# Kernel tuning notes

Hardware: AMD Instinct MI355X
Metric: run time of the kernel (lower is better)

## Reference

```python
import jax, jax.numpy as jnp
import numpy as np
from jax import lax

NUM_SKETCH = 3
BN_EPS = 1e-5


def setup_inputs() -> dict:
    key = jax.random.key(0)
    ks = jax.random.split(key, 8)
    B, C, H, W = 32, 128, 64, 64
    D = C // 4  # comp_rate = 4
    k = 3
    x = jax.random.normal(ks[0], (B, C, H, W), dtype=jnp.float32)
    fan = C * k * k
    w1 = jax.random.normal(ks[1], (C, C, k, k), dtype=jnp.float32) / np.sqrt(fan)
    w2 = jax.random.normal(ks[2], (C, C, k, k), dtype=jnp.float32) / np.sqrt(fan)
    gamma1 = jnp.ones((C,), jnp.float32); beta1 = jnp.zeros((C,), jnp.float32)
    gamma2 = jnp.ones((C,), jnp.float32); beta2 = jnp.zeros((C,), jnp.float32)
    # count-sketch hash matrices: hs[j] is (D, C), each column c has a single 1
    idx = jax.random.randint(ks[3], (NUM_SKETCH, C), 0, D)
    hs = jax.nn.one_hot(idx, D, dtype=jnp.float32).transpose(0, 2, 1)  # (3, D, C)
    ss = (jax.random.randint(ks[4], (NUM_SKETCH, C), 0, 2) * 2 - 1).astype(jnp.float32)  # (3, C) signs
    return {"x": x, "w1": w1, "w2": w2, "gamma1": gamma1, "beta1": beta1,
            "gamma2": gamma2, "beta2": beta2, "hs": hs, "ss": ss}


def _sketch_conv_unsketch(x, w, hs, ss):
    # w: (Co, Ci, k, k); hs: (J, D, Co); ss: (J, Co)
    Co, Ci, k, _ = w.shape
    J, D, _ = hs.shape
    B, _, H, W = x.shape
    wf = w.reshape(Co, -1)  # (Co, M)
    # sketched weights per sketch j: h_j @ (wf * s_j[:, None])
    w_sk = jnp.einsum('jdc,jc,cm->jdm', hs, ss, wf).reshape(J * D, Ci, k, k)
    # one conv with J*D output channels (padding=1, stride=1 hardcoded in source)
    y = lax.conv_general_dilated(x, w_sk, window_strides=(1, 1),
                                 padding=[(1, 1), (1, 1)],
                                 dimension_numbers=('NCHW', 'OIHW', 'NCHW'))
    y = y.reshape(B, J, D, H, W)
    # unsketch activations: h_j^T @ y_j, then sign scale (num_s=1 so inner median is identity)
    y_un = jnp.einsum('jdc,bjdhw->jbchw', hs, y) * ss[:, None, :, None, None]
    return jnp.median(y_un, axis=0)  # median over the 3 sketches -> (B, Co, H, W)


def _bn_relu(y, gamma, beta):
    # BatchNorm2d in training mode: biased batch stats over (N, H, W)
    mean = jnp.mean(y, axis=(0, 2, 3), keepdims=True)
    var = jnp.var(y, axis=(0, 2, 3), keepdims=True)
    yhat = (y - mean) * lax.rsqrt(var + BN_EPS)
    return jax.nn.relu(yhat * gamma[None, :, None, None] + beta[None, :, None, None])


def reference(x, w1, w2, gamma1, beta1, gamma2, beta2, hs, ss):
    residual = x
    out1 = _bn_relu(_sketch_conv_unsketch(x, w1, hs, ss), gamma1, beta1)
    del out1  # faithful to source bug: second conv loop uses x, discarding out1
    out = _bn_relu(_sketch_conv_unsketch(x, w2, hs, ss), gamma2, beta2)
    return out + residual
```

## Files before the change

### kernel.cpp

```cpp
#include <hip/hip_runtime.h>
#include <stdint.h>

typedef __bf16 bf16x8 __attribute__((ext_vector_type(8)));
typedef float  f32x4  __attribute__((ext_vector_type(4)));

static constexpr int Bn = 32, Cn = 128, Hn = 64, Wn = 64, HWn = 4096;
static constexpr size_t OFF_XT    = 0;
static constexpr size_t OFF_WF    = 33554432;
static constexpr size_t OFF_IDX   = 33775616;
static constexpr size_t OFF_M     = 33777152;
static constexpr size_t OFF_STATS = 67331584;
static constexpr size_t OFF_ZERO  = 67364352;

__device__ __forceinline__ unsigned short f32_to_bf16(float f) {
    union { float f; unsigned u; } v; v.f = f;
    unsigned u = v.u;
    return (unsigned short)((u + 0x7FFFu + ((u >> 16) & 1u)) >> 16);
}
__device__ __forceinline__ float bf16_to_f32(unsigned short h) {
    union { unsigned u; float f; } v; v.u = ((unsigned)h) << 16;
    return v.f;
}
__device__ __forceinline__ float bf_lo(unsigned w) {
    union { unsigned u; float f; } v; v.u = w << 16; return v.f;
}
__device__ __forceinline__ float bf_hi(unsigned w) {
    union { unsigned u; float f; } v; v.u = w & 0xffff0000u; return v.f;
}
__device__ __forceinline__ float med3(float z0, float z1, float z2) {
    float lo = fminf(z0, z1), hi = fmaxf(z0, z1);
    return fmaxf(lo, fminf(hi, z2));
}
__device__ __forceinline__ void gload_lds16(const unsigned short* g, unsigned short* l) {
    __builtin_amdgcn_global_load_lds(
        (const __attribute__((address_space(1))) unsigned int*)(const void*)g,
        (__attribute__((address_space(3))) unsigned int*)(void*)l,
        16, 0, 0);
}

__global__ __launch_bounds__(256) void k_prep(const float* __restrict__ x,
                                              unsigned short* __restrict__ xT,
                                              const float* __restrict__ w2,
                                              const float* __restrict__ hs,
                                              const float* __restrict__ ss,
                                              unsigned short* __restrict__ wf,
                                              int* __restrict__ idx,
                                              float* __restrict__ stats32,
                                              float* __restrict__ zerop) {
    __shared__ __align__(16) unsigned char smraw[20480];
    int t = threadIdx.x;
    if (blockIdx.x < 432) {
        int*   idxs = (int*)smraw;
        float* sss  = (float*)(smraw + 1536);
        for (int i = t; i < 384; i += 256) {
            int j = i >> 7, c = i & 127;
            int found = 0;
#pragma unroll
            for (int d = 0; d < 32; ++d)
                if (hs[(j * 32 + d) * 128 + c] > 0.5f) found = d;
            idxs[i] = found;
            sss[i]  = ss[i];
        }
        __syncthreads();
        int f = blockIdx.x * 256 + t;
        int jj   = f & 7;
        int lane = (f >> 3) & 63;
        int nt   = (f >> 9) % 6;
        int qt   = f / (512 * 6);
        int tp   = qt % 9;
        int q    = qt / 9;
        int k  = ((lane >> 4) << 3) + jj;
        int ci = q * 32 + k;
        int n  = nt * 16 + (lane & 15);
        int j = n >> 5, d = n & 31;
        const int*   ij = idxs + j * 128;
        const float* sj = sss  + j * 128;
        float sum = 0.f;
        for (int c = 0; c < 128; ++c)
            if (ij[c] == d) sum += sj[c] * w2[(c * 128 + ci) * 9 + tp];
        wf[f] = f32_to_bf16(sum);
    } else if (blockIdx.x == 432) {
        for (int i = t; i < 384; i += 256) {
            int j = i >> 7, c = i & 127;
            int found = 0;
            for (int d = 0; d < 32; ++d)
                if (hs[(j * 32 + d) * 128 + c] > 0.5f) found = d;
            idx[i] = found;
        }
        for (int i = t; i < 8192; i += 256) stats32[i] = 0.f;
        if (t < 64) zerop[t] = 0.f;
    } else {
        unsigned short* sm = (unsigned short*)smraw;
        int blk = blockIdx.x - 433;
        int pt = blk & 15, q = (blk >> 4) & 3, b = blk >> 6;
        int p0 = pt * 256;
        const float* xp = x + ((size_t)(b * Cn + q * 32) * HWn) + p0 + t;
#pragma unroll
        for (int cil = 0; cil < 32; ++cil)
            sm[t * 40 + cil] = f32_to_bf16(xp[(size_t)cil * HWn]);
        __syncthreads();
        uint4* dst = (uint4*)xT;
#pragma unroll
        for (int pass = 0; pass < 4; ++pass) {
            int pix = pass * 64 + (t >> 2);
            int ch  = t & 3;
            dst[(size_t)(b * HWn + p0 + pix) * 16 + q * 4 + ch] = *(const uint4*)(&sm[pix * 40 + ch * 8]);
        }
    }
}

__global__ __launch_bounds__(256, 2) void k_conv(const unsigned short* __restrict__ xT,
                                                 const unsigned short* __restrict__ wf,
                                                 const int* __restrict__ idx,
                                                 const float* __restrict__ ss,
                                                 unsigned short* __restrict__ m_out,
                                                 float* __restrict__ stats32,
                                                 const unsigned short* __restrict__ zerop) {
    __shared__ __align__(16) unsigned short sm[33792];
    int tid  = threadIdx.x;
    int blk  = blockIdx.x;
    int tile = blk & 31, b = blk >> 5;
    int ty0  = tile * 2;
    int wv   = tid >> 6, lane = tid & 63;
    int quad = lane >> 4, l15 = lane & 15;
    int row_l = wv >> 1, nh = wv & 1;

    {
        const unsigned short* xb = xT + (size_t)b * (HWn * 128);
#pragma unroll
        for (int i = 0; i < 17; ++i) {
            if (i < 16 || tid < 128) {
                int k  = i * 256 + tid;
                int r  = k >> 4, cl = k & 15;
                int sl = cl ^ (r & 7);
                int hy = r / 66, hx = r - hy * 66;
                int gy = ty0 + hy - 1, gx = hx - 1;
                const unsigned short* src = (gy >= 0 && gy < 64 && gx >= 0 && gx < 64)
                        ? (xb + ((size_t)(gy * 64 + gx) * 128 + sl * 8)) : zerop;
                gload_lds16(src, &sm[(size_t)k * 8]);
            }
        }
    }
    __syncthreads();

    f32x4 acc[4][3];
#pragma unroll
    for (int a = 0; a < 4; ++a)
#pragma unroll
        for (int nb = 0; nb < 3; ++nb) acc[a][nb] = (f32x4){0.f, 0.f, 0.f, 0.f};

    const unsigned short* wl = wf + (size_t)(nh * 3) * 512 + lane * 8;

    for (int q = 0; q < 4; ++q) {
#pragma unroll
        for (int tp = 0; tp < 9; ++tp) {
            int dy = tp / 3, dx = tp % 3;
            bf16x8 bfr[3];
            const unsigned short* wb = wl + (size_t)((q * 9 + tp) * 6) * 512;
#pragma unroll
            for (int nb = 0; nb < 3; ++nb)
                bfr[nb] = *(const bf16x8*)(wb + nb * 512);
            int rb = (row_l + dy) * 66 + l15 + dx;
            int sw = ((4 * q + quad) ^ (rb & 7)) * 16;
            bf16x8 afr[4];
#pragma unroll
            for (int mq = 0; mq < 4; ++mq)
                afr[mq] = *(const bf16x8*)((const unsigned char*)sm + (rb + mq * 16) * 256 + sw);
            __builtin_amdgcn_s_setprio(1);
#pragma unroll
            for (int mq = 0; mq < 4; ++mq)
#pragma unroll
                for (int nb = 0; nb < 3; ++nb)
                    acc[mq][nb] = __builtin_amdgcn_mfma_f32_16x16x32_bf16(afr[mq], bfr[nb], acc[mq][nb], 0, 0, 0);
            __builtin_amdgcn_s_setprio(0);
        }
    }

    __syncthreads();
#pragma unroll
    for (int mq = 0; mq < 4; ++mq)
#pragma unroll
        for (int nb = 0; nb < 3; ++nb) {
            int ch = nh * 48 + nb * 16 + l15;
            int px = row_l * 64 + mq * 16 + quad * 4;
            ushort4 v;
            v.x = f32_to_bf16(acc[mq][nb][0]);
            v.y = f32_to_bf16(acc[mq][nb][1]);
            v.z = f32_to_bf16(acc[mq][nb][2]);
            v.w = f32_to_bf16(acc[mq][nb][3]);
            *(ushort4*)(&sm[ch * 136 + px]) = v;
        }
    __syncthreads();
    unsigned short* mpb = m_out + (size_t)b * Cn * HWn + tile * 128 + l15 * 8;
    float* stp = stats32 + (blk & 31) * 256;
#pragma unroll 2
    for (int i = 0; i < 8; ++i) {
        int c = wv * 32 + i * 4 + quad;
        int r0 = idx[c], r1 = 32 + idx[128 + c], r2 = 64 + idx[256 + c];
        float sg0 = ss[c], sg1 = ss[128 + c], sg2 = ss[256 + c];
        uint4 w0 = *(const uint4*)(&sm[r0 * 136 + l15 * 8]);
        uint4 w1 = *(const uint4*)(&sm[r1 * 136 + l15 * 8]);
        uint4 w2v = *(const uint4*)(&sm[r2 * 136 + l15 * 8]);
        const unsigned* u0 = (const unsigned*)&w0;
        const unsigned* u1 = (const unsigned*)&w1;
        const unsigned* u2 = (const unsigned*)&w2v;
        uint4 R;
        unsigned* rw = (unsigned*)&R;
        float s = 0.f, s2 = 0.f;
#pragma unroll
        for (int e = 0; e < 4; ++e) {
            float mlo = med3(sg0 * bf_lo(u0[e]), sg1 * bf_lo(u1[e]), sg2 * bf_lo(u2[e]));
            float mhi = med3(sg0 * bf_hi(u0[e]), sg1 * bf_hi(u1[e]), sg2 * bf_hi(u2[e]));
            s  += mlo + mhi;
            s2 += mlo * mlo + mhi * mhi;
            rw[e] = (unsigned)f32_to_bf16(mlo) | ((unsigned)f32_to_bf16(mhi) << 16);
        }
        *(uint4*)(mpb + (size_t)c * HWn) = R;
#pragma unroll
        for (int o = 8; o > 0; o >>= 1) { s += __shfl_xor(s, o); s2 += __shfl_xor(s2, o); }
        if (l15 == 0) { atomicAdd(&stp[c], s); atomicAdd(&stp[128 + c], s2); }
    }
}

__global__ __launch_bounds__(256) void k_apply(const unsigned short* __restrict__ m,
                                               const float* __restrict__ x,
                                               const float* __restrict__ stats32,
                                               const float* __restrict__ gamma,
                                               const float* __restrict__ beta,
                                               float* __restrict__ out) {
    __shared__ float co[2];
    int tid = threadIdx.x;
    int i4 = blockIdx.x * 256 + tid;
    int c = (blockIdx.x >> 2) & 127;
    if (tid < 64) {
        float v = stats32[(tid & 31) * 256 + ((tid >> 5) << 7) + c];
#pragma unroll
        for (int o = 16; o > 0; o >>= 1) v += __shfl_xor(v, o);
        if ((tid & 31) == 0) co[tid >> 5] = v;
    }
    __syncthreads();
    const float N = 131072.f;
    float mean = co[0] / N;
    float var  = co[1] / N - mean * mean;
    float sc   = gamma[c] * rsqrtf(var + 1e-5f);
    float sh   = beta[c] - mean * sc;
    ushort4 mv = ((const ushort4*)m)[i4];
    float4  xv = ((const float4*)x)[i4];
    float4 o;
    o.x = fmaxf(bf16_to_f32(mv.x) * sc + sh, 0.f) + xv.x;
    o.y = fmaxf(bf16_to_f32(mv.y) * sc + sh, 0.f) + xv.y;
    o.z = fmaxf(bf16_to_f32(mv.z) * sc + sh, 0.f) + xv.z;
    o.w = fmaxf(bf16_to_f32(mv.w) * sc + sh, 0.f) + xv.w;
    ((float4*)out)[i4] = o;
}

extern "C" void kernel_launch(void* const* d_in, const int* in_sizes, int n_in,
                              void* d_out, int out_size, void* d_ws, size_t ws_size,
                              hipStream_t stream) {
    const float* x      = (const float*)d_in[0];
    const float* w2     = (const float*)d_in[2];
    const float* gamma2 = (const float*)d_in[5];
    const float* beta2  = (const float*)d_in[6];
    const float* hs     = (const float*)d_in[7];
    const float* ss     = (const float*)d_in[8];
    float* out = (float*)d_out;

    char* ws = (char*)d_ws;
    unsigned short* xT  = (unsigned short*)(ws + OFF_XT);
    unsigned short* wfp = (unsigned short*)(ws + OFF_WF);
    int*            idp = (int*)(ws + OFF_IDX);
    unsigned short* mp  = (unsigned short*)(ws + OFF_M);
    float*          st  = (float*)(ws + OFF_STATS);
    float*          zp  = (float*)(ws + OFF_ZERO);

    k_prep<<<2481, 256, 0, stream>>>(x, xT, w2, hs, ss, wfp, idp, st, zp);
    k_conv<<<1024, 256, 0, stream>>>(xT, wfp, idp, ss, mp, st, (const unsigned short*)zp);
    k_apply<<<16384, 256, 0, stream>>>(mp, x, st, gamma2, beta2, out);
}
```

Baseline: 209.7 us.

## Double-buffer conv input halo per channel quarter and change xT layout

Changes the transposed input layout so each 32-channel quarter is stored contiguously, then stages only one quarter of the halo tile into shared memory at a time, double-buffered so the next quarter loads while MFMAs run on the current one. This halves shared memory per block, allowing launch bounds to request 3 blocks per CU instead of 2. The swizzle is adapted to 64-byte pixel rows. It adds a sync per quarter and smaller, more numerous loads.

New measurement: 205.7 us. Within noise of the previous version (-1.9%).

```diff
diff --git a/kernel.cpp b/kernel.cpp
--- a/kernel.cpp
+++ b/kernel.cpp
@@ -88,7 +88,7 @@
             idx[i] = found;
         }
         for (int i = t; i < 8192; i += 256) stats32[i] = 0.f;
-        if (t < 64) zerop[t] = 0.f;
+        if (t < 32) zerop[t] = 0.f;
     } else {
         unsigned short* sm = (unsigned short*)smraw;
         int blk = blockIdx.x - 433;
@@ -99,24 +99,24 @@
         for (int cil = 0; cil < 32; ++cil)
             sm[t * 40 + cil] = f32_to_bf16(xp[(size_t)cil * HWn]);
         __syncthreads();
-        uint4* dst = (uint4*)xT;
+        uint4* dst = (uint4*)(xT + ((size_t)(b * 4 + q) * HWn + p0) * 32);
 #pragma unroll
         for (int pass = 0; pass < 4; ++pass) {
             int pix = pass * 64 + (t >> 2);
             int ch  = t & 3;
-            dst[(size_t)(b * HWn + p0 + pix) * 16 + q * 4 + ch] = *(const uint4*)(&sm[pix * 40 + ch * 8]);
-        }
-    }
-}
-
-__global__ __launch_bounds__(256, 2) void k_conv(const unsigned short* __restrict__ xT,
+            dst[pix * 4 + ch] = *(const uint4*)(&sm[pix * 40 + ch * 8]);
+        }
+    }
+}
+
+__global__ __launch_bounds__(256, 3) void k_conv(const unsigned short* __restrict__ xT,
                                                  const unsigned short* __restrict__ wf,
                                                  const int* __restrict__ idx,
                                                  const float* __restrict__ ss,
                                                  unsigned short* __restrict__ m_out,
                                                  float* __restrict__ stats32,
                                                  const unsigned short* __restrict__ zerop) {
-    __shared__ __align__(16) unsigned short sm[33792];
+    __shared__ __align__(16) unsigned short sm[16896];
     int tid  = threadIdx.x;
     int blk  = blockIdx.x;
     int tile = blk & 31, b = blk >> 5;
@@ -125,33 +125,48 @@
     int quad = lane >> 4, l15 = lane & 15;
     int row_l = wv >> 1, nh = wv & 1;
 
-    {
-        const unsigned short* xb = xT + (size_t)b * (HWn * 128);
-#pragma unroll
-        for (int i = 0; i < 17; ++i) {
-            if (i < 16 || tid < 128) {
-                int k  = i * 256 + tid;
-                int r  = k >> 4, cl = k & 15;
-                int sl = cl ^ (r & 7);
-                int hy = r / 66, hx = r - hy * 66;
-                int gy = ty0 + hy - 1, gx = hx - 1;
-                const unsigned short* src = (gy >= 0 && gy < 64 && gx >= 0 && gx < 64)
-                        ? (xb + ((size_t)(gy * 64 + gx) * 128 + sl * 8)) : zerop;
-                gload_lds16(src, &sm[(size_t)k * 8]);
-            }
-        }
-    }
+    int goff[5];
+#pragma unroll
+    for (int i = 0; i < 5; ++i) {
+        int k = (i < 4) ? (tid + i * 256) : (tid + 1024);
+        bool act = (i < 4) || (tid < 32);
+        int r  = k >> 2;
+        int cl = (k & 3) ^ ((r >> 1) & 3);
+        int hy = r / 66, hx = r - hy * 66;
+        int gy = ty0 + hy - 1, gx = hx - 1;
+        goff[i] = (act && gy >= 0 && gy < 64 && gx >= 0 && gx < 64)
+                ? ((gy * 64 + gx) * 32 + cl * 8) : -1;
+    }
+
+    f32x4 acc[4][3];
+#pragma unroll
+    for (int a = 0; a < 4; ++a)
+#pragma unroll
+        for (int nb = 0; nb < 3; ++nb) acc[a][nb] = (f32x4){0.f, 0.f, 0.f, 0.f};
+
+    const unsigned short* wl = wf + (size_t)(nh * 3) * 512 + lane * 8;
+
+#define STAGE(qv, half)                                                               \
+    {                                                                                 \
+        const unsigned short* xq = xT + (size_t)(b * 4 + (qv)) * (HWn * 32);          \
+        unsigned short* dstb = sm + (half) * 8448;                                    \
+        _Pragma("unroll")                                                             \
+        for (int i = 0; i < 4; ++i) {                                                 \
+            int k = tid + i * 256;                                                    \
+            gload_lds16((goff[i] >= 0) ? (xq + goff[i]) : zerop, dstb + k * 8);       \
+        }                                                                             \
+        if (tid < 32) {                                                               \
+            int k = tid + 1024;                                                       \
+            gload_lds16((goff[4] >= 0) ? (xq + goff[4]) : zerop, dstb + k * 8);       \
+        }                                                                             \
+    }
+
+    STAGE(0, 0)
     __syncthreads();
 
-    f32x4 acc[4][3];
-#pragma unroll
-    for (int a = 0; a < 4; ++a)
-#pragma unroll
-        for (int nb = 0; nb < 3; ++nb) acc[a][nb] = (f32x4){0.f, 0.f, 0.f, 0.f};
-
-    const unsigned short* wl = wf + (size_t)(nh * 3) * 512 + lane * 8;
-
     for (int q = 0; q < 4; ++q) {
+        const unsigned char* cur = (const unsigned char*)(sm + (q & 1) * 8448);
+        if (q < 3) STAGE(q + 1, (q + 1) & 1)
 #pragma unroll
         for (int tp = 0; tp < 9; ++tp) {
             int dy = tp / 3, dx = tp % 3;
@@ -160,12 +175,14 @@
 #pragma unroll
             for (int nb = 0; nb < 3; ++nb)
                 bfr[nb] = *(const bf16x8*)(wb + nb * 512);
-            int rb = (row_l + dy) * 66 + l15 + dx;
-            int sw = ((4 * q + quad) ^ (rb & 7)) * 16;
             bf16x8 afr[4];
 #pragma unroll
-            for (int mq = 0; mq < 4; ++mq)
-                afr[mq] = *(const bf16x8*)((const unsigned char*)sm + (rb + mq * 16) * 256 + sw);
+            for (int mq = 0; mq < 4; ++mq) {
+                int pix = (row_l + dy) * 66 + mq * 16 + l15 + dx;
+                int byo = (pix << 6) + (quad << 4);
+                byo ^= ((byo >> 7) & 3) << 4;
+                afr[mq] = *(const bf16x8*)(cur + byo);
+            }
             __builtin_amdgcn_s_setprio(1);
 #pragma unroll
             for (int mq = 0; mq < 4; ++mq)
@@ -174,9 +191,10 @@
                     acc[mq][nb] = __builtin_amdgcn_mfma_f32_16x16x32_bf16(afr[mq], bfr[nb], acc[mq][nb], 0, 0, 0);
             __builtin_amdgcn_s_setprio(0);
         }
-    }
-
-    __syncthreads();
+        __syncthreads();
+    }
+#undef STAGE
+
 #pragma unroll
     for (int mq = 0; mq < 4; ++mq)
 #pragma unroll
```
